# Kernel tuning notes

Hardware: AMD Instinct MI355X
Metric: run time of the kernel (lower is better)

The kernel has to match this reference:

```python
import jax, jax.numpy as jnp
import numpy as np

N = 50000   # nodes
E = 800000  # edges
F = 256     # input features
H = 256     # hidden units
L = 128     # n_labels
EPS = 1e-5


def setup_inputs():
    key = jax.random.key(0)
    ks = jax.random.split(key, 17)
    s = 0.05
    return {
        "features": jax.random.normal(ks[0], (N, F), jnp.float32),
        "edge_vals": jax.random.uniform(ks[1], (E,), jnp.float32),
        "W1": jax.random.normal(ks[2], (F, H), jnp.float32) * s,
        "db1": jax.random.normal(ks[3], (H,), jnp.float32) * s,
        "b1": jax.random.normal(ks[4], (H,), jnp.float32) * s,
        "g1": jax.random.uniform(ks[5], (H,), jnp.float32, 0.5, 1.5),
        "be1": jax.random.normal(ks[6], (H,), jnp.float32) * s,
        "W2": jax.random.normal(ks[7], (H, H), jnp.float32) * s,
        "b2": jax.random.normal(ks[8], (H,), jnp.float32) * s,
        "g2": jax.random.uniform(ks[9], (H,), jnp.float32, 0.5, 1.5),
        "be2": jax.random.normal(ks[10], (H,), jnp.float32) * s,
        "Wf": jax.random.normal(ks[11], (H, L), jnp.float32) * s,
        "bf": jax.random.normal(ks[12], (L,), jnp.float32) * s,
        "edge_rows": jax.random.randint(ks[13], (E,), 0, N, jnp.int32),
        "edge_cols": jax.random.randint(ks[14], (E,), 0, N, jnp.int32),
        "idx": jax.random.randint(ks[15], (N // 2,), 0, N, jnp.int32),
    }


def _spmm(edge_vals, rows, cols, x):
    # out[i] = sum_{(i,j) in E} A[i,j] * x[j]  (COO sparse @ dense)
    return jax.ops.segment_sum(edge_vals[:, None] * x[cols], rows, num_segments=N)


def _bn(x, gamma, beta):
    # training-mode BatchNormalization: batch (population) stats over nodes
    m = jnp.mean(x, axis=0)
    v = jnp.var(x, axis=0)
    return (x - m) * jax.lax.rsqrt(v + EPS) * gamma + beta


def reference(features, edge_vals, W1, db1, b1, g1, be1, W2, b2, g2, be2, Wf, bf,
              edge_rows, edge_cols, idx):
    # layer 1 (Dense has bias only for l == 0)
    h = features @ W1 + db1
    h = _spmm(edge_vals, edge_rows, edge_cols, h) + b1
    h = jax.nn.relu(_bn(h, g1, be1))
    # layer 2 (no dense bias)
    h = h @ W2
    h = _spmm(edge_vals, edge_rows, edge_cols, h) + b2
    h = jax.nn.relu(_bn(h, g2, be2))
    # dropout = identity (deterministic baseline); final dense head
    out = h @ Wf + bf
    return out[idx]
```

## Files before the change

### kernel.cpp

```cpp
#include <hip/hip_runtime.h>
#include <stdint.h>

#define NN 50000
#define EE 800000
#define FF 256
#define HH 256
#define LL 128
#define SBLK 1024

typedef __bf16 bf16x8 __attribute__((ext_vector_type(8)));
typedef float  f32x4  __attribute__((ext_vector_type(4)));

typedef __attribute__((address_space(1))) unsigned int uint_as1;
typedef __attribute__((address_space(3))) unsigned int uint_as3;

__device__ __forceinline__ unsigned short f2bf(float f) {
  union { float f; unsigned int u; } v; v.f = f;
  unsigned int u = v.u;
  u += 0x7FFFu + ((u >> 16) & 1u);
  return (unsigned short)(u >> 16);
}

__device__ __forceinline__ float bf2f(unsigned short u) {
  union { unsigned int u; float f; } v;
  v.u = ((unsigned int)u) << 16;
  return v.f;
}

__device__ __forceinline__ f32x4 bf4_to_f32(ushort4 u) {
  f32x4 r;
  r.x = bf2f(u.x); r.y = bf2f(u.y); r.z = bf2f(u.z); r.w = bf2f(u.w);
  return r;
}

__device__ __forceinline__ void gload_lds16(const void* g, void* l) {
  __builtin_amdgcn_global_load_lds((const uint_as1*)g, (uint_as3*)l, 16, 0, 0);
}

__global__ __launch_bounds__(256) void k_setup(const int* __restrict__ erows,
                                               int* __restrict__ cnt,
                                               const float* __restrict__ features,
                                               unsigned short* __restrict__ Xb,
                                               const float* __restrict__ W1,
                                               unsigned short* __restrict__ W1t,
                                               const float* __restrict__ W2,
                                               unsigned short* __restrict__ W2t,
                                               const float* __restrict__ Wf,
                                               unsigned short* __restrict__ Wft) {
  __shared__ float tl[64 * 65];
  int b = blockIdx.x, t = threadIdx.x;
  if (b < 3125) {
    int i = b * 256 + t;
    if (i < EE) atomicAdd(&cnt[erows[i]], 1);
  } else if (b < 15625) {
    int i = (b - 3125) * 256 + t;
    f32x4 x = ((const f32x4*)features)[i];
    ushort4 o;
    o.x = f2bf(x.x); o.y = f2bf(x.y); o.z = f2bf(x.z); o.w = f2bf(x.w);
    ((ushort4*)Xb)[i] = o;
  } else {
    int tt = b - 15625;
    const float* in;
    unsigned short* out;
    int Nin, k0, n0;
    if (tt < 16) {
      in = W1; out = W1t; Nin = HH;
      k0 = (tt >> 2) * 64; n0 = (tt & 3) * 64;
    } else if (tt < 32) {
      in = W2; out = W2t; Nin = HH;
      tt -= 16; k0 = (tt >> 2) * 64; n0 = (tt & 3) * 64;
    } else {
      in = Wf; out = Wft; Nin = LL;
      tt -= 32; k0 = (tt >> 1) * 64; n0 = (tt & 1) * 64;
    }
#pragma unroll
    for (int j = 0; j < 16; ++j) {
      int idx = j * 256 + t;
      int r = idx >> 6, c = idx & 63;
      tl[r * 65 + c] = in[(size_t)(k0 + r) * Nin + n0 + c];
    }
    __syncthreads();
#pragma unroll
    for (int j = 0; j < 16; ++j) {
      int idx = j * 256 + t;
      int r = idx >> 6, c = idx & 63;
      out[(size_t)(n0 + r) * HH + k0 + c] = f2bf(tl[c * 65 + r]);
    }
  }
}

__global__ __launch_bounds__(256) void k_alloc(const int* __restrict__ cnt,
                                               int* __restrict__ cursor,
                                               int* __restrict__ total, int n) {
  int i = blockIdx.x * 256 + threadIdx.x;
  int lane = threadIdx.x & 63;
  int c = (i < n) ? cnt[i] : 0;
  int incl = c;
#pragma unroll
  for (int off = 1; off < 64; off <<= 1) {
    int v = __shfl_up(incl, off, 64);
    if (lane >= off) incl += v;
  }
  int excl = incl - c;
  int wtot = __shfl(incl, 63, 64);
  int base = 0;
  if (lane == 0) base = atomicAdd(total, wtot);
  base = __shfl(base, 0, 64);
  if (i < n) cursor[i] = base + excl;
}

__global__ __launch_bounds__(256, 3) void k_l1(const unsigned short* __restrict__ A,
                                               const unsigned short* __restrict__ Bt,
                                               const float* __restrict__ bias,
                                               unsigned short* __restrict__ C,
                                               int M, int K, int Nn,
                                               const int* __restrict__ rows,
                                               const int* __restrict__ cols,
                                               const float* __restrict__ vals,
                                               int* __restrict__ cursor,
                                               unsigned int* __restrict__ csr, int E) {
  __shared__ unsigned short lA[128 * 64];
  __shared__ unsigned short lB[128 * 64];
  const int b = blockIdx.x;
  const int tid = threadIdx.x;
  if (b & 1) {
    for (int i = (b >> 1) * 256 + tid; i < E; i += 782 * 256) {
      int p = atomicAdd(&cursor[rows[i]], 1);
      csr[p] = ((unsigned int)cols[i] << 16) | (unsigned int)f2bf(vals[i]);
    }
    return;
  }
  const int gb = b >> 1;
  const int m0 = (gb % 391) * 128, n0 = (gb / 391) * 128;
  const int wave = tid >> 6, lane = tid & 63;
  const int wm = (wave >> 1) * 64, wn = (wave & 1) * 64;
  const int lhi = lane >> 4, llo = lane & 15;
  const int srow = lane >> 3;
  const int scol = (lane & 7) * 8;
  const unsigned short *pA[4], *pB[4];
#pragma unroll
  for (int j = 0; j < 4; ++j) {
    int base = (wave * 4 + j) * 8 + srow;
    int ar = m0 + base;
    ar = ar < M ? ar : 0;
    pA[j] = A + (size_t)ar * K + scol;
    pB[j] = Bt + (size_t)(n0 + base) * K + scol;
  }
  f32x4 zero = {0.f, 0.f, 0.f, 0.f};
  f32x4 acc[4][4];
#pragma unroll
  for (int i = 0; i < 4; ++i)
#pragma unroll
    for (int j = 0; j < 4; ++j) acc[i][j] = zero;
  for (int k0 = 0; k0 < K; k0 += 64) {
#pragma unroll
    for (int j = 0; j < 4; ++j) {
      gload_lds16(pA[j] + k0, lA + (wave * 4 + j) * 8 * 64);
      gload_lds16(pB[j] + k0, lB + (wave * 4 + j) * 8 * 64);
    }
    __syncthreads();
    bf16x8 af[2][4], bfv[2][4];
#pragma unroll
    for (int ks = 0; ks < 2; ++ks) {
#pragma unroll
      for (int mt = 0; mt < 4; ++mt)
        af[ks][mt] = *(const bf16x8*)(lA + (wm + mt * 16 + llo) * 64 + ks * 32 + lhi * 8);
#pragma unroll
      for (int nt = 0; nt < 4; ++nt)
        bfv[ks][nt] = *(const bf16x8*)(lB + (wn + nt * 16 + llo) * 64 + ks * 32 + lhi * 8);
    }
#pragma unroll
    for (int ks = 0; ks < 2; ++ks)
#pragma unroll
      for (int mt = 0; mt < 4; ++mt)
#pragma unroll
        for (int nt = 0; nt < 4; ++nt)
          acc[mt][nt] = __builtin_amdgcn_mfma_f32_16x16x32_bf16(af[ks][mt], bfv[ks][nt], acc[mt][nt], 0, 0, 0);
    __syncthreads();
  }
#pragma unroll
  for (int nt = 0; nt < 4; ++nt) {
    int cn = n0 + wn + nt * 16 + llo;
    float bv = bias[cn];
#pragma unroll
    for (int mt = 0; mt < 4; ++mt) {
      int cm0 = m0 + wm + mt * 16 + lhi * 4;
#pragma unroll
      for (int r = 0; r < 4; ++r) {
        int cm = cm0 + r;
        if (cm < M) C[(size_t)cm * Nn + cn] = f2bf(acc[mt][nt][r] + bv);
      }
    }
  }
}

__global__ __launch_bounds__(256) void k_spmm(const unsigned short* __restrict__ X,
                                              const int* __restrict__ endp,
                                              const int* __restrict__ cnt,
                                              const unsigned int* __restrict__ csr,
                                              unsigned short* __restrict__ Y, int n) {
  int row = blockIdx.x * 4 + (threadIdx.x >> 6);
  int lane = threadIdx.x & 63;
  if (row >= n) return;
  int e = endp[row];
  int s = e - cnt[row];
  f32x4 a0 = {0.f, 0.f, 0.f, 0.f};
  f32x4 a1 = a0, a2 = a0, a3 = a0;
  int p = s;
  int e4 = s + ((e - s) & ~3);
  for (; p < e4; p += 4) {
    unsigned int c0 = csr[p + 0], c1 = csr[p + 1], c2 = csr[p + 2], c3 = csr[p + 3];
    ushort4 x0 = ((const ushort4*)(X + (size_t)(c0 >> 16) * HH))[lane];
    ushort4 x1 = ((const ushort4*)(X + (size_t)(c1 >> 16) * HH))[lane];
    ushort4 x2 = ((const ushort4*)(X + (size_t)(c2 >> 16) * HH))[lane];
    ushort4 x3 = ((const ushort4*)(X + (size_t)(c3 >> 16) * HH))[lane];
    a0 += bf2f((unsigned short)c0) * bf4_to_f32(x0);
    a1 += bf2f((unsigned short)c1) * bf4_to_f32(x1);
    a2 += bf2f((unsigned short)c2) * bf4_to_f32(x2);
    a3 += bf2f((unsigned short)c3) * bf4_to_f32(x3);
  }
  for (; p < e; ++p) {
    unsigned int c0 = csr[p];
    ushort4 x0 = ((const ushort4*)(X + (size_t)(c0 >> 16) * HH))[lane];
    a0 += bf2f((unsigned short)c0) * bf4_to_f32(x0);
  }
  f32x4 a = (a0 + a1) + (a2 + a3);
  ushort4 o;
  o.x = f2bf(a.x); o.y = f2bf(a.y); o.z = f2bf(a.z); o.w = f2bf(a.w);
  ((ushort4*)(Y + (size_t)row * HH))[lane] = o;
}

__global__ __launch_bounds__(256) void k_bnstats(const unsigned short* __restrict__ X,
                                                 float* __restrict__ part, int n) {
  __shared__ float red[4][64][9];
  const int w = threadIdx.x >> 6, l = threadIdx.x & 63;
  f32x4 s = {0.f, 0.f, 0.f, 0.f}, s2 = {0.f, 0.f, 0.f, 0.f};
  for (int r = blockIdx.x * 4 + w; r < n; r += gridDim.x * 4) {
    f32x4 v = bf4_to_f32(((const ushort4*)(X + (size_t)r * HH))[l]);
    s += v;
    s2 += v * v;
  }
#pragma unroll
  for (int j = 0; j < 4; ++j) { red[w][l][j] = s[j]; red[w][l][4 + j] = s2[j]; }
  __syncthreads();
  if (threadIdx.x < 64) {
    int ll = threadIdx.x;
#pragma unroll
    for (int j = 0; j < 8; ++j) {
      float v = red[0][ll][j] + red[1][ll][j] + red[2][ll][j] + red[3][ll][j];
      int c = ll * 4 + (j & 3);
      part[((j < 4) ? 0 : (SBLK * 256)) + blockIdx.x * 256 + c] = v;
    }
  }
}

__global__ __launch_bounds__(256) void k_bnred(const float* __restrict__ part,
                                               float* __restrict__ sums) {
  int c = threadIdx.x;
  int stat = blockIdx.x >> 3, chunk = blockIdx.x & 7;
  const float* p = part + stat * (SBLK * 256) + chunk * 128 * 256;
  float s0 = 0.f, s1 = 0.f, s2 = 0.f, s3 = 0.f;
  for (int b = 0; b < 128; b += 4) {
    s0 += p[(b + 0) * 256 + c];
    s1 += p[(b + 1) * 256 + c];
    s2 += p[(b + 2) * 256 + c];
    s3 += p[(b + 3) * 256 + c];
  }
  atomicAdd(&sums[stat * HH + c], (s0 + s1) + (s2 + s3));
}

__global__ __launch_bounds__(256) void k_bnrc(const unsigned short* __restrict__ X,
                                              const float* __restrict__ sums,
                                              const float* __restrict__ g,
                                              const float* __restrict__ be,
                                              unsigned short* __restrict__ out, int n4) {
  __shared__ float sc[HH], sh[HH];
  int t = threadIdx.x;
  {
    float inv = 1.f / (float)NN;
    float mean = sums[t] * inv;
    float var = sums[HH + t] * inv - mean * mean;
    float s = g[t] * rsqrtf(var + 1e-5f);
    sc[t] = s;
    sh[t] = be[t] - mean * s;
  }
  __syncthreads();
  for (int i = blockIdx.x * 256 + t; i < n4; i += gridDim.x * 256) {
    f32x4 x = bf4_to_f32(((const ushort4*)X)[i]);
    int c0 = (i * 4) & (HH - 1);
    ushort4 o;
    o.x = f2bf(fmaxf(x.x * sc[c0 + 0] + sh[c0 + 0], 0.f));
    o.y = f2bf(fmaxf(x.y * sc[c0 + 1] + sh[c0 + 1], 0.f));
    o.z = f2bf(fmaxf(x.z * sc[c0 + 2] + sh[c0 + 2], 0.f));
    o.w = f2bf(fmaxf(x.w * sc[c0 + 3] + sh[c0 + 3], 0.f));
    ((ushort4*)out)[i] = o;
  }
}

__global__ __launch_bounds__(256) void k_bnrc_pack(const unsigned short* __restrict__ X,
                                                   const float* __restrict__ sums,
                                                   const float* __restrict__ g,
                                                   const float* __restrict__ be,
                                                   const int* __restrict__ idx,
                                                   unsigned short* __restrict__ out) {
  __shared__ float sc[HH], sh[HH];
  int t = threadIdx.x;
  {
    float inv = 1.f / (float)NN;
    float mean = sums[t] * inv;
    float var = sums[HH + t] * inv - mean * mean;
    float s = g[t] * rsqrtf(var + 1e-5f);
    sc[t] = s;
    sh[t] = be[t] - mean * s;
  }
  __syncthreads();
  int i = blockIdx.x * 256 + t;
  int orow = i >> 6;
  int c0 = (i & 63) * 4;
  int irow = idx[orow];
  f32x4 x = bf4_to_f32(*(const ushort4*)(X + (size_t)irow * HH + c0));
  ushort4 o;
  o.x = f2bf(fmaxf(x.x * sc[c0 + 0] + sh[c0 + 0], 0.f));
  o.y = f2bf(fmaxf(x.y * sc[c0 + 1] + sh[c0 + 1], 0.f));
  o.z = f2bf(fmaxf(x.z * sc[c0 + 2] + sh[c0 + 2], 0.f));
  o.w = f2bf(fmaxf(x.w * sc[c0 + 3] + sh[c0 + 3], 0.f));
  ((ushort4*)out)[i] = o;
}

template <int OUTB>
__global__ __launch_bounds__(256, 3) void k_gemm(const unsigned short* __restrict__ A,
                                                 const unsigned short* __restrict__ Bt,
                                                 const float* __restrict__ bias,
                                                 void* __restrict__ Cv,
                                                 int M, int K, int Nn) {
  __shared__ unsigned short lA[128 * 64];
  __shared__ unsigned short lB[128 * 64];
  const int tid = threadIdx.x;
  const int wave = tid >> 6, lane = tid & 63;
  const int m0 = blockIdx.x * 128, n0 = blockIdx.y * 128;
  const int wm = (wave >> 1) * 64, wn = (wave & 1) * 64;
  const int lhi = lane >> 4, llo = lane & 15;
  const int srow = lane >> 3;
  const int scol = (lane & 7) * 8;
  const unsigned short *pA[4], *pB[4];
#pragma unroll
  for (int j = 0; j < 4; ++j) {
    int base = (wave * 4 + j) * 8 + srow;
    int ar = m0 + base;
    ar = ar < M ? ar : 0;
    pA[j] = A + (size_t)ar * K + scol;
    pB[j] = Bt + (size_t)(n0 + base) * K + scol;
  }
  f32x4 zero = {0.f, 0.f, 0.f, 0.f};
  f32x4 acc[4][4];
#pragma unroll
  for (int i = 0; i < 4; ++i)
#pragma unroll
    for (int j = 0; j < 4; ++j) acc[i][j] = zero;
  for (int k0 = 0; k0 < K; k0 += 64) {
#pragma unroll
    for (int j = 0; j < 4; ++j) {
      gload_lds16(pA[j] + k0, lA + (wave * 4 + j) * 8 * 64);
      gload_lds16(pB[j] + k0, lB + (wave * 4 + j) * 8 * 64);
    }
    __syncthreads();
    bf16x8 af[2][4], bfv[2][4];
#pragma unroll
    for (int ks = 0; ks < 2; ++ks) {
#pragma unroll
      for (int mt = 0; mt < 4; ++mt)
        af[ks][mt] = *(const bf16x8*)(lA + (wm + mt * 16 + llo) * 64 + ks * 32 + lhi * 8);
#pragma unroll
      for (int nt = 0; nt < 4; ++nt)
        bfv[ks][nt] = *(const bf16x8*)(lB + (wn + nt * 16 + llo) * 64 + ks * 32 + lhi * 8);
    }
#pragma unroll
    for (int ks = 0; ks < 2; ++ks)
#pragma unroll
      for (int mt = 0; mt < 4; ++mt)
#pragma unroll
        for (int nt = 0; nt < 4; ++nt)
          acc[mt][nt] = __builtin_amdgcn_mfma_f32_16x16x32_bf16(af[ks][mt], bfv[ks][nt], acc[mt][nt], 0, 0, 0);
    __syncthreads();
  }
#pragma unroll
  for (int nt = 0; nt < 4; ++nt) {
    int cn = n0 + wn + nt * 16 + llo;
    float bv = bias ? bias[cn] : 0.f;
#pragma unroll
    for (int mt = 0; mt < 4; ++mt) {
      int cm0 = m0 + wm + mt * 16 + lhi * 4;
#pragma unroll
      for (int r = 0; r < 4; ++r) {
        int cm = cm0 + r;
        if (cm < M) {
          float v = acc[mt][nt][r] + bv;
          if (OUTB)
            ((unsigned short*)Cv)[(size_t)cm * Nn + cn] = f2bf(v);
          else
            ((float*)Cv)[(size_t)cm * Nn + cn] = v;
        }
      }
    }
  }
}

extern "C" void kernel_launch(void* const* d_in, const int* in_sizes, int n_in,
                              void* d_out, int out_size, void* d_ws, size_t ws_size,
                              hipStream_t stream) {
  const float* features = (const float*)d_in[0];
  const float* edge_vals = (const float*)d_in[1];
  const float* W1 = (const float*)d_in[2];
  const float* db1 = (const float*)d_in[3];
  const float* g1 = (const float*)d_in[5];
  const float* be1 = (const float*)d_in[6];
  const float* W2 = (const float*)d_in[7];
  const float* g2 = (const float*)d_in[9];
  const float* be2 = (const float*)d_in[10];
  const float* Wf = (const float*)d_in[11];
  const float* bfb = (const float*)d_in[12];
  const int* erows = (const int*)d_in[13];
  const int* ecols = (const int*)d_in[14];
  const int* idx = (const int*)d_in[15];
  const int M3 = in_sizes[15];
  (void)n_in; (void)out_size; (void)ws_size;

  char* ws = (char*)d_ws;
  size_t off = 0;
  auto alloc = [&](size_t bytes) -> void* {
    void* p = (void*)(ws + off);
    off += (bytes + 255) & ~(size_t)255;
    return p;
  };
  unsigned short* Xb = (unsigned short*)alloc((size_t)NN * HH * 2);
  unsigned short* Ab = (unsigned short*)alloc((size_t)NN * HH * 2);
  unsigned short* Yb = (unsigned short*)alloc((size_t)NN * HH * 2);
  unsigned short* Pb = (unsigned short*)alloc((size_t)25000 * HH * 2);
  unsigned short* W1t = (unsigned short*)alloc((size_t)FF * HH * 2);
  unsigned short* W2t = (unsigned short*)alloc((size_t)HH * HH * 2);
  unsigned short* Wft = (unsigned short*)alloc((size_t)HH * LL * 2);
  int* cursor = (int*)alloc((size_t)NN * 4);
  int* cnt = (int*)alloc((size_t)NN * 4);
  unsigned int* csr = (unsigned int*)alloc((size_t)EE * 4);
  float* part = (float*)alloc((size_t)2 * SBLK * 256 * 4);
  float* stats = (float*)alloc(4 * HH * 4 + 256);
  float* sums1 = stats;
  float* sums2 = stats + 2 * HH;
  int* total = (int*)(stats + 4 * HH);

  hipMemsetAsync(cnt, 0, (size_t)NN * 4, stream);
  hipMemsetAsync(stats, 0, 4 * HH * 4 + 256, stream);

  k_setup<<<15665, 256, 0, stream>>>(erows, cnt, features, Xb, W1, W1t, W2, W2t, Wf, Wft);
  k_alloc<<<(NN + 255) / 256, 256, 0, stream>>>(cnt, cursor, total, NN);

  k_l1<<<1564, 256, 0, stream>>>(Xb, W1t, db1, Ab, NN, FF, HH,
                                 erows, ecols, edge_vals, cursor, csr, EE);
  k_spmm<<<(NN + 3) / 4, 256, 0, stream>>>(Ab, cursor, cnt, csr, Yb, NN);
  k_bnstats<<<SBLK, 256, 0, stream>>>(Yb, part, NN);
  k_bnred<<<16, 256, 0, stream>>>(part, sums1);
  k_bnrc<<<2048, 256, 0, stream>>>(Yb, sums1, g1, be1, Xb, NN * HH / 4);

  k_gemm<1><<<dim3((NN + 127) / 128, HH / 128), 256, 0, stream>>>(Xb, W2t, nullptr, Ab, NN, HH, HH);
  k_spmm<<<(NN + 3) / 4, 256, 0, stream>>>(Ab, cursor, cnt, csr, Yb, NN);
  k_bnstats<<<SBLK, 256, 0, stream>>>(Yb, part, NN);
  k_bnred<<<16, 256, 0, stream>>>(part, sums2);
  k_bnrc_pack<<<(M3 * 64) / 256, 256, 0, stream>>>(Yb, sums2, g2, be2, idx, Pb);

  k_gemm<0><<<dim3((M3 + 127) / 128, LL / 128), 256, 0, stream>>>(Pb, Wft, bfb, d_out, M3, HH, LL);
}
```

Baseline: 433.7 us.

## Split SpMM feature columns into slices and spread edges across lanes

The SpMM kernel now gives each block one 32-column slice of 16 rows. Within each wave, 8 lane groups each walk a different edge, and each group's 8 lanes load 4 columns apiece. Partial sums are then combined with cross-lane shuffles. Nontemporal loads and stores are used for the CSR stream and the output. The goal is more memory-level parallelism on each row and better cache locality per column slice. The cost is that the CSR entries are re-read 8 times, once per slice, and extra shuffle work is added.

```diff
diff --git a/kernel.cpp b/kernel.cpp
--- a/kernel.cpp
+++ b/kernel.cpp
@@ -10,6 +10,7 @@
 
 typedef __bf16 bf16x8 __attribute__((ext_vector_type(8)));
 typedef float  f32x4  __attribute__((ext_vector_type(4)));
+typedef unsigned int u32x2 __attribute__((ext_vector_type(2)));
 
 typedef __attribute__((address_space(1))) unsigned int uint_as1;
 typedef __attribute__((address_space(3))) unsigned int uint_as3;
@@ -199,35 +200,40 @@
                                               const int* __restrict__ cnt,
                                               const unsigned int* __restrict__ csr,
                                               unsigned short* __restrict__ Y, int n) {
-  int row = blockIdx.x * 4 + (threadIdx.x >> 6);
-  int lane = threadIdx.x & 63;
-  if (row >= n) return;
-  int e = endp[row];
-  int s = e - cnt[row];
-  f32x4 a0 = {0.f, 0.f, 0.f, 0.f};
-  f32x4 a1 = a0, a2 = a0, a3 = a0;
-  int p = s;
-  int e4 = s + ((e - s) & ~3);
-  for (; p < e4; p += 4) {
-    unsigned int c0 = csr[p + 0], c1 = csr[p + 1], c2 = csr[p + 2], c3 = csr[p + 3];
-    ushort4 x0 = ((const ushort4*)(X + (size_t)(c0 >> 16) * HH))[lane];
-    ushort4 x1 = ((const ushort4*)(X + (size_t)(c1 >> 16) * HH))[lane];
-    ushort4 x2 = ((const ushort4*)(X + (size_t)(c2 >> 16) * HH))[lane];
-    ushort4 x3 = ((const ushort4*)(X + (size_t)(c3 >> 16) * HH))[lane];
-    a0 += bf2f((unsigned short)c0) * bf4_to_f32(x0);
-    a1 += bf2f((unsigned short)c1) * bf4_to_f32(x1);
-    a2 += bf2f((unsigned short)c2) * bf4_to_f32(x2);
-    a3 += bf2f((unsigned short)c3) * bf4_to_f32(x3);
-  }
-  for (; p < e; ++p) {
-    unsigned int c0 = csr[p];
-    ushort4 x0 = ((const ushort4*)(X + (size_t)(c0 >> 16) * HH))[lane];
-    a0 += bf2f((unsigned short)c0) * bf4_to_f32(x0);
-  }
-  f32x4 a = (a0 + a1) + (a2 + a3);
-  ushort4 o;
-  o.x = f2bf(a.x); o.y = f2bf(a.y); o.z = f2bf(a.z); o.w = f2bf(a.w);
-  ((ushort4*)(Y + (size_t)row * HH))[lane] = o;
+  const int slice = blockIdx.x & 7;
+  const int rb = blockIdx.x >> 3;
+  const int wave = threadIdx.x >> 6, lane = threadIdx.x & 63;
+  const int eg = lane >> 3;
+  const int cl = lane & 7;
+  const int coloff = slice * 32 + cl * 4;
+  const unsigned short* Xs = X + coloff;
+#pragma unroll
+  for (int r = 0; r < 4; ++r) {
+    const int row = rb * 16 + wave * 4 + r;
+    if (row >= n) continue;
+    const int e = endp[row];
+    int q = e - cnt[row] + eg;
+    f32x4 acc = {0.f, 0.f, 0.f, 0.f};
+    for (; q < e; q += 8) {
+      const unsigned int cv = __builtin_nontemporal_load(csr + q);
+      const float val = bf2f((unsigned short)cv);
+      const ushort4 x = *(const ushort4*)(Xs + ((size_t)(cv >> 16) << 8));
+      acc += val * bf4_to_f32(x);
+    }
+#pragma unroll
+    for (int m = 8; m < 64; m <<= 1) {
+      acc.x += __shfl_xor(acc.x, m, 64);
+      acc.y += __shfl_xor(acc.y, m, 64);
+      acc.z += __shfl_xor(acc.z, m, 64);
+      acc.w += __shfl_xor(acc.w, m, 64);
+    }
+    if (eg == 0) {
+      u32x2 o;
+      o.x = ((unsigned int)f2bf(acc.y) << 16) | (unsigned int)f2bf(acc.x);
+      o.y = ((unsigned int)f2bf(acc.w) << 16) | (unsigned int)f2bf(acc.z);
+      __builtin_nontemporal_store(o, (u32x2*)(Y + (size_t)row * HH + coloff));
+    }
+  }
 }
 
 __global__ __launch_bounds__(256) void k_bnstats(const unsigned short* __restrict__ X,
@@ -456,13 +462,13 @@
 
   k_l1<<<1564, 256, 0, stream>>>(Xb, W1t, db1, Ab, NN, FF, HH,
                                  erows, ecols, edge_vals, cursor, csr, EE);
-  k_spmm<<<(NN + 3) / 4, 256, 0, stream>>>(Ab, cursor, cnt, csr, Yb, NN);
+  k_spmm<<<3125 * 8, 256, 0, stream>>>(Ab, cursor, cnt, csr, Yb, NN);
   k_bnstats<<<SBLK, 256, 0, stream>>>(Yb, part, NN);
   k_bnred<<<16, 256, 0, stream>>>(part, sums1);
   k_bnrc<<<2048, 256, 0, stream>>>(Yb, sums1, g1, be1, Xb, NN * HH / 4);
 
   k_gemm<1><<<dim3((NN + 127) / 128, HH / 128), 256, 0, stream>>>(Xb, W2t, nullptr, Ab, NN, HH, HH);
-  k_spmm<<<(NN + 3) / 4, 256, 0, stream>>>(Ab, cursor, cnt, csr, Yb, NN);
+  k_spmm<<<3125 * 8, 256, 0, stream>>>(Ab, cursor, cnt, csr, Yb, NN);
   k_bnstats<<<SBLK, 256, 0, stream>>>(Yb, part, NN);
   k_bnred<<<16, 256, 0, stream>>>(part, sums2);
   k_bnrc_pack<<<(M3 * 64) / 256, 256, 0, stream>>>(Yb, sums2, g2, be2, idx, Pb);
```

Result: slower. 678.1 us (+56.4%).

## Pad CSR rows to multiples of eight and stage block edges in LDS

Applied to the files above, without the earlier changes.

Each CSR row is padded to a multiple of 8 entries, and the buffer is zeroed so padded entries contribute nothing (column 0, value 0). The SpMM kernel then cooperatively loads the block's contiguous CSR slice into shared memory with vectorized nontemporal loads and processes eight gathers per iteration with eight accumulators, removing the scalar tail loop and raising memory-level parallelism. CSR writes and loads use nontemporal hints. The cost is an extra memset of about 4.8MB, wasted gathers of row 0 for padding entries, and a block-wide sync.

```diff
diff --git a/kernel.cpp b/kernel.cpp
--- a/kernel.cpp
+++ b/kernel.cpp
@@ -7,9 +7,13 @@
 #define HH 256
 #define LL 128
 #define SBLK 1024
+#define CSRCAP 1200128
+#define SCAP 512
 
 typedef __bf16 bf16x8 __attribute__((ext_vector_type(8)));
 typedef float  f32x4  __attribute__((ext_vector_type(4)));
+typedef unsigned int u32x2 __attribute__((ext_vector_type(2)));
+typedef unsigned int u32x4 __attribute__((ext_vector_type(4)));
 
 typedef __attribute__((address_space(1))) unsigned int uint_as1;
 typedef __attribute__((address_space(3))) unsigned int uint_as3;
@@ -94,7 +98,7 @@
                                                int* __restrict__ total, int n) {
   int i = blockIdx.x * 256 + threadIdx.x;
   int lane = threadIdx.x & 63;
-  int c = (i < n) ? cnt[i] : 0;
+  int c = (i < n) ? ((cnt[i] + 7) & ~7) : 0;
   int incl = c;
 #pragma unroll
   for (int off = 1; off < 64; off <<= 1) {
@@ -126,7 +130,8 @@
   if (b & 1) {
     for (int i = (b >> 1) * 256 + tid; i < E; i += 782 * 256) {
       int p = atomicAdd(&cursor[rows[i]], 1);
-      csr[p] = ((unsigned int)cols[i] << 16) | (unsigned int)f2bf(vals[i]);
+      __builtin_nontemporal_store(
+          ((unsigned int)cols[i] << 16) | (unsigned int)f2bf(vals[i]), &csr[p]);
     }
     return;
   }
@@ -199,32 +204,56 @@
                                               const int* __restrict__ cnt,
                                               const unsigned int* __restrict__ csr,
                                               unsigned short* __restrict__ Y, int n) {
-  int row = blockIdx.x * 4 + (threadIdx.x >> 6);
-  int lane = threadIdx.x & 63;
+  __shared__ unsigned int lcsr[SCAP];
+  const int r0 = blockIdx.x * 4;
+  const int tid = threadIdx.x;
+  const int wave = tid >> 6, lane = tid & 63;
+
+  const int rlast = (r0 + 3 < n) ? (r0 + 3) : (n - 1);
+  const int s0 = endp[r0] - cnt[r0];
+  const int clast = cnt[rlast];
+  const int send = (endp[rlast] - clast) + ((clast + 7) & ~7);
+  const int len0 = send - s0;
+  const int len = len0 < SCAP ? len0 : SCAP;
+  for (int j = tid * 4; j < len; j += 1024)
+    *(u32x4*)(lcsr + j) = __builtin_nontemporal_load((const u32x4*)(csr + s0 + j));
+  __syncthreads();
+
+  const int row = r0 + wave;
   if (row >= n) return;
-  int e = endp[row];
-  int s = e - cnt[row];
-  f32x4 a0 = {0.f, 0.f, 0.f, 0.f};
-  f32x4 a1 = a0, a2 = a0, a3 = a0;
-  int p = s;
-  int e4 = s + ((e - s) & ~3);
-  for (; p < e4; p += 4) {
-    unsigned int c0 = csr[p + 0], c1 = csr[p + 1], c2 = csr[p + 2], c3 = csr[p + 3];
-    ushort4 x0 = ((const ushort4*)(X + (size_t)(c0 >> 16) * HH))[lane];
-    ushort4 x1 = ((const ushort4*)(X + (size_t)(c1 >> 16) * HH))[lane];
-    ushort4 x2 = ((const ushort4*)(X + (size_t)(c2 >> 16) * HH))[lane];
-    ushort4 x3 = ((const ushort4*)(X + (size_t)(c3 >> 16) * HH))[lane];
-    a0 += bf2f((unsigned short)c0) * bf4_to_f32(x0);
-    a1 += bf2f((unsigned short)c1) * bf4_to_f32(x1);
-    a2 += bf2f((unsigned short)c2) * bf4_to_f32(x2);
-    a3 += bf2f((unsigned short)c3) * bf4_to_f32(x3);
-  }
-  for (; p < e; ++p) {
-    unsigned int c0 = csr[p];
-    ushort4 x0 = ((const ushort4*)(X + (size_t)(c0 >> 16) * HH))[lane];
-    a0 += bf2f((unsigned short)c0) * bf4_to_f32(x0);
-  }
-  f32x4 a = (a0 + a1) + (a2 + a3);
+  const int c = cnt[row];
+  int q = endp[row] - c;
+  const int qe = q + ((c + 7) & ~7);
+
+  f32x4 a0 = {0.f, 0.f, 0.f, 0.f}, a1 = a0, a2 = a0, a3 = a0;
+  f32x4 a4 = a0, a5 = a0, a6 = a0, a7 = a0;
+  auto gat = [&](unsigned int cv) -> ushort4 {
+    return ((const ushort4*)(X + ((size_t)(cv >> 16)) * HH))[lane];
+  };
+  auto oct = [&](u32x4 ca, u32x4 cb) {
+    const ushort4 x0 = gat(ca.x), x1 = gat(ca.y), x2 = gat(ca.z), x3 = gat(ca.w);
+    const ushort4 x4 = gat(cb.x), x5 = gat(cb.y), x6 = gat(cb.z), x7 = gat(cb.w);
+    a0 += bf2f((unsigned short)ca.x) * bf4_to_f32(x0);
+    a1 += bf2f((unsigned short)ca.y) * bf4_to_f32(x1);
+    a2 += bf2f((unsigned short)ca.z) * bf4_to_f32(x2);
+    a3 += bf2f((unsigned short)ca.w) * bf4_to_f32(x3);
+    a4 += bf2f((unsigned short)cb.x) * bf4_to_f32(x4);
+    a5 += bf2f((unsigned short)cb.y) * bf4_to_f32(x5);
+    a6 += bf2f((unsigned short)cb.z) * bf4_to_f32(x6);
+    a7 += bf2f((unsigned short)cb.w) * bf4_to_f32(x7);
+  };
+
+  if (len0 <= len) {
+    const unsigned int* lp = lcsr + (q - s0);
+    for (; q < qe; q += 8, lp += 8)
+      oct(*(const u32x4*)(lp), *(const u32x4*)(lp + 4));
+  } else {
+    for (; q < qe; q += 8)
+      oct(__builtin_nontemporal_load((const u32x4*)(csr + q)),
+          __builtin_nontemporal_load((const u32x4*)(csr + q + 4)));
+  }
+
+  const f32x4 a = ((a0 + a1) + (a2 + a3)) + ((a4 + a5) + (a6 + a7));
   ushort4 o;
   o.x = f2bf(a.x); o.y = f2bf(a.y); o.z = f2bf(a.z); o.w = f2bf(a.w);
   ((ushort4*)(Y + (size_t)row * HH))[lane] = o;
@@ -441,7 +470,7 @@
   unsigned short* Wft = (unsigned short*)alloc((size_t)HH * LL * 2);
   int* cursor = (int*)alloc((size_t)NN * 4);
   int* cnt = (int*)alloc((size_t)NN * 4);
-  unsigned int* csr = (unsigned int*)alloc((size_t)EE * 4);
+  unsigned int* csr = (unsigned int*)alloc((size_t)CSRCAP * 4);
   float* part = (float*)alloc((size_t)2 * SBLK * 256 * 4);
   float* stats = (float*)alloc(4 * HH * 4 + 256);
   float* sums1 = stats;
@@ -449,6 +478,7 @@
   int* total = (int*)(stats + 4 * HH);
 
   hipMemsetAsync(cnt, 0, (size_t)NN * 4, stream);
+  hipMemsetAsync(csr, 0, (size_t)CSRCAP * 4, stream);
   hipMemsetAsync(stats, 0, 4 * HH * 4 + 256, stream);
 
   k_setup<<<15665, 256, 0, stream>>>(erows, cnt, features, Xb, W1, W1t, W2, W2t, Wf, Wft);
```

New measurement: 437.6 us. No clear change (+0.9%).
